# Optimization experiments

Hardware: AMD Instinct MI355X
Metric: run time of the kernel (lower is better)

Reference implementation:

```python
import jax, jax.numpy as jnp
import numpy as np

OUT_W, OUT_L, OUT_H = 7, 7, 7   # output_size
SR = 2                          # sampling_ratio (samples per bin per axis)


def setup_inputs() -> dict:
    key = jax.random.key(0)
    k1, k2, k3, k4, k5 = jax.random.split(key, 5)
    B, C, W, L, H = 2, 128, 64, 64, 64
    N = 128
    inp = jax.random.normal(k1, (B, C, W, L, H), jnp.float32)
    bidx = jax.random.randint(k2, (N,), 0, B).astype(jnp.float32)
    ctr = jax.random.uniform(k3, (N, 3), minval=8.0, maxval=56.0)
    size = jax.random.uniform(k4, (N, 3), minval=8.0, maxval=32.0)
    theta = jax.random.uniform(k5, (N, 1), minval=-np.pi, maxval=np.pi)
    rois = jnp.concatenate([bidx[:, None], ctr, size, theta], axis=1)  # [N,8]
    return {"input": inp, "rois": rois, "spatial_scale": jnp.float32(1.0)}


def _trilinear_gather(vol, b, x, y, z):
    # vol: [B,W,L,H,C]; b: [N]; x,y,z: [N,PW,PL,PH] float coords.
    B, W, L, H, C = vol.shape
    valid = (x > -1.0) & (x < W) & (y > -1.0) & (y < L) & (z > -1.0) & (z < H)
    x = jnp.clip(x, 0.0, W - 1.0)
    y = jnp.clip(y, 0.0, L - 1.0)
    z = jnp.clip(z, 0.0, H - 1.0)
    x0 = jnp.floor(x).astype(jnp.int32)
    y0 = jnp.floor(y).astype(jnp.int32)
    z0 = jnp.floor(z).astype(jnp.int32)
    x1 = jnp.minimum(x0 + 1, W - 1)
    y1 = jnp.minimum(y0 + 1, L - 1)
    z1 = jnp.minimum(z0 + 1, H - 1)
    lx = x - x0; hx = 1.0 - lx
    ly = y - y0; hy = 1.0 - ly
    lz = z - z0; hz = 1.0 - lz
    bb = b[:, None, None, None]

    def g(xi, yi, zi):
        return vol[bb, xi, yi, zi]  # [N,PW,PL,PH,C]

    out = (g(x0, y0, z0) * (hx * hy * hz)[..., None]
           + g(x1, y0, z0) * (lx * hy * hz)[..., None]
           + g(x0, y1, z0) * (hx * ly * hz)[..., None]
           + g(x1, y1, z0) * (lx * ly * hz)[..., None]
           + g(x0, y0, z1) * (hx * hy * lz)[..., None]
           + g(x1, y0, z1) * (lx * hy * lz)[..., None]
           + g(x0, y1, z1) * (hx * ly * lz)[..., None]
           + g(x1, y1, z1) * (lx * ly * lz)[..., None])
    return out * valid[..., None]


def _axis_offsets(size, nbins):
    # size: [N]; returns [N, nbins*SR] local coords centered at 0.
    binw = size / nbins
    i = jnp.arange(nbins * SR, dtype=jnp.float32)
    return (-size * 0.5)[:, None] + (i[None, :] + 0.5) * (binw / SR)[:, None]


def roi_align_rotated_3d(input, rois, spatial_scale):
    B, C, W, L, H = input.shape
    vol = jnp.transpose(input, (0, 2, 3, 4, 1))  # [B,W,L,H,C]
    b = rois[:, 0].astype(jnp.int32)
    ctr = rois[:, 1:4] * spatial_scale           # cx,cy,cz
    size = rois[:, 4:7] * spatial_scale          # w,l,h
    theta = rois[:, 7]
    N = rois.shape[0]

    xx = _axis_offsets(size[:, 0], OUT_W)[:, :, None, None]  # [N,PW,1,1]
    yy = _axis_offsets(size[:, 1], OUT_L)[:, None, :, None]  # [N,1,PL,1]
    zz = _axis_offsets(size[:, 2], OUT_H)[:, None, None, :]  # [N,1,1,PH]

    c = jnp.cos(theta)[:, None, None, None]
    s = jnp.sin(theta)[:, None, None, None]
    # rotate sample offsets about z-axis, then shift to ROI center
    x = c * xx - s * yy + ctr[:, 0][:, None, None, None]
    y = s * xx + c * yy + ctr[:, 1][:, None, None, None]
    z = jnp.broadcast_to(zz + ctr[:, 2][:, None, None, None],
                         (N, OUT_W * SR, OUT_L * SR, OUT_H * SR))
    x = jnp.broadcast_to(x, z.shape)
    y = jnp.broadcast_to(y, z.shape)

    vals = _trilinear_gather(vol, b, x, y, z)  # [N,PW,PL,PH,C]
    vals = vals.reshape(N, OUT_W, SR, OUT_L, SR, OUT_H, SR, C)
    pooled = vals.mean(axis=(2, 4, 6))          # [N,OW,OL,OH,C]
    return jnp.transpose(pooled, (0, 4, 1, 2, 3))  # [N,C,OW,OL,OH]


def reference(input, rois, spatial_scale):
    return roi_align_rotated_3d(input, rois, spatial_scale)
```

## Files before the change

kernel.cpp:

```cpp
#include <hip/hip_runtime.h>

#define OUT_W 7
#define OUT_L 7
#define OUT_H 7
#define SR 2
#define CDIM 128
#define WDIM 64
#define LDIM 64
#define HDIM 64
#define VOLSZ (WDIM * LDIM * HDIM)
#define CPB 2

typedef float f4 __attribute__((ext_vector_type(4)));

#define GLOAD(dst, p) asm volatile("global_load_dwordx4 %0, %1, off" : "=v"(dst) : "v"(p))

struct ColInfo { int b00, b10, b01, b11; float w00, w10, w01, w11; };

__global__ __launch_bounds__(384) void roi_align_rot3d_kernel(
    const float* __restrict__ input, const float* __restrict__ rois,
    const float* __restrict__ scale_ptr, float* __restrict__ out, int N)
{
    __shared__ ColInfo cols[OUT_W * SR * OUT_L * SR];
    __shared__ alignas(16) float zw[OUT_H][8];
    __shared__ int zb4s[OUT_H];

    const int nwg = N * (CDIM / CPB);
    const int q = nwg >> 3, rr = nwg & 7;
    const int xcd = blockIdx.x & 7;
    const int idx_in = blockIdx.x >> 3;
    const int w = (xcd < rr ? xcd * (q + 1) : rr * (q + 1) + (xcd - rr) * q) + idx_in;
    const int cp = w / N;
    const int n  = w - cp * N;
    const int c0 = cp * CPB;
    const int t = threadIdx.x;

    const float scale = scale_ptr[0];
    const float* r = rois + (size_t)n * 8;
    const int   b  = (int)r[0];
    const float cx = r[1] * scale, cy = r[2] * scale, cz = r[3] * scale;
    const float sx = r[4] * scale, sy = r[5] * scale, szv = r[6] * scale;
    const float th = r[7];
    const float ct = cosf(th), st = sinf(th);

    if (t < 196) {
        const int isx = t / 14, isy = t - isx * 14;
        const float xx = -0.5f * sx + ((float)isx + 0.5f) * (sx * (1.0f / 14.0f));
        const float yy = -0.5f * sy + ((float)isy + 0.5f) * (sy * (1.0f / 14.0f));
        float x = ct * xx - st * yy + cx;
        float y = st * xx + ct * yy + cy;
        const bool v = (x > -1.0f) && (x < (float)WDIM) && (y > -1.0f) && (y < (float)LDIM);
        x = fminf(fmaxf(x, 0.0f), (float)(WDIM - 1));
        y = fminf(fmaxf(y, 0.0f), (float)(LDIM - 1));
        const int x0 = (int)floorf(x);
        const int y0 = (int)floorf(y);
        const int x1 = min(x0 + 1, WDIM - 1);
        const int y1 = min(y0 + 1, LDIM - 1);
        const float lx = x - (float)x0, ly = y - (float)y0;
        const float hx = 1.0f - lx, hy = 1.0f - ly;
        const float vm = v ? 1.0f : 0.0f;
        cols[t].b00 = x0 * (LDIM * HDIM) + y0 * HDIM;
        cols[t].b10 = x1 * (LDIM * HDIM) + y0 * HDIM;
        cols[t].b01 = x0 * (LDIM * HDIM) + y1 * HDIM;
        cols[t].b11 = x1 * (LDIM * HDIM) + y1 * HDIM;
        cols[t].w00 = hx * hy * vm; cols[t].w10 = lx * hy * vm;
        cols[t].w01 = hx * ly * vm; cols[t].w11 = lx * ly * vm;
    } else if (t < 196 + OUT_H) {
        const int oh = t - 196;
        float w8[8];
        #pragma unroll
        for (int k = 0; k < 8; ++k) w8[k] = 0.0f;
        int zb4 = 0;
        #pragma unroll
        for (int dz = 0; dz < 2; ++dz) {
            const int s = oh * 2 + dz;
            const float zraw = -0.5f * szv + ((float)s + 0.5f) * (szv * (1.0f / 14.0f)) + cz;
            const bool v = (zraw > -1.0f) && (zraw < (float)HDIM);
            const float z = fminf(fmaxf(zraw, 0.0f), (float)(HDIM - 1));
            const int z0 = (int)floorf(z);
            const int z1 = min(z0 + 1, HDIM - 1);
            const float lz = z - (float)z0, hz = 1.0f - lz;
            const float vm = v ? 1.0f : 0.0f;
            if (dz == 0) zb4 = min(z0 & ~3, HDIM - 8);
            w8[z0 - zb4] += hz * vm;
            w8[z1 - zb4] += lz * vm;
        }
        zb4s[oh] = zb4;
        #pragma unroll
        for (int k = 0; k < 8; ++k) zw[oh][k] = w8[k];
    }
    __syncthreads();

    if (t >= 343) return;
    const int ow = t / 49;
    const int rem = t - ow * 49;
    const int ol = rem / 7;
    const int oh = rem - ol * 7;

    const float4 zwa = *(const float4*)&zw[oh][0];
    const float4 zwb = *(const float4*)&zw[oh][4];
    const int zb4 = zb4s[oh];

    const float* __restrict__ p =
        input + ((size_t)(b * CDIM + c0)) * (size_t)VOLSZ;

    float acc0 = 0.0f, acc1 = 0.0f;

    #pragma unroll
    for (int dx = 0; dx < 2; ++dx) {
        #pragma unroll
        for (int dy = 0; dy < 2; ++dy) {
            const ColInfo col = cols[(ow * 2 + dx) * 14 + (ol * 2 + dy)];
            const float* a0 = p + (col.b00 + zb4);
            const float* a1 = p + (col.b10 + zb4);
            const float* a2 = p + (col.b01 + zb4);
            const float* a3 = p + (col.b11 + zb4);
            const float* b0 = a0 + VOLSZ;
            const float* b1 = a1 + VOLSZ;
            const float* b2 = a2 + VOLSZ;
            const float* b3 = a3 + VOLSZ;
            f4 r00, r01, r02, r03, r04, r05, r06, r07;
            f4 r08, r09, r10, r11, r12, r13, r14, r15;
            GLOAD(r00, a0); GLOAD(r01, a0 + 4);
            GLOAD(r02, a1); GLOAD(r03, a1 + 4);
            GLOAD(r04, a2); GLOAD(r05, a2 + 4);
            GLOAD(r06, a3); GLOAD(r07, a3 + 4);
            GLOAD(r08, b0); GLOAD(r09, b0 + 4);
            GLOAD(r10, b1); GLOAD(r11, b1 + 4);
            GLOAD(r12, b2); GLOAD(r13, b2 + 4);
            GLOAD(r14, b3); GLOAD(r15, b3 + 4);
            asm volatile("s_waitcnt vmcnt(0)"
                : "+v"(r00), "+v"(r01), "+v"(r02), "+v"(r03),
                  "+v"(r04), "+v"(r05), "+v"(r06), "+v"(r07),
                  "+v"(r08), "+v"(r09), "+v"(r10), "+v"(r11),
                  "+v"(r12), "+v"(r13), "+v"(r14), "+v"(r15));
            const float v00 = zwa.x*r00.x + zwa.y*r00.y + zwa.z*r00.z + zwa.w*r00.w
                            + zwb.x*r01.x + zwb.y*r01.y + zwb.z*r01.z + zwb.w*r01.w;
            const float v10 = zwa.x*r02.x + zwa.y*r02.y + zwa.z*r02.z + zwa.w*r02.w
                            + zwb.x*r03.x + zwb.y*r03.y + zwb.z*r03.z + zwb.w*r03.w;
            const float v01 = zwa.x*r04.x + zwa.y*r04.y + zwa.z*r04.z + zwa.w*r04.w
                            + zwb.x*r05.x + zwb.y*r05.y + zwb.z*r05.z + zwb.w*r05.w;
            const float v11 = zwa.x*r06.x + zwa.y*r06.y + zwa.z*r06.z + zwa.w*r06.w
                            + zwb.x*r07.x + zwb.y*r07.y + zwb.z*r07.z + zwb.w*r07.w;
            acc0 += col.w00 * v00 + col.w10 * v10 + col.w01 * v01 + col.w11 * v11;
            const float u00 = zwa.x*r08.x + zwa.y*r08.y + zwa.z*r08.z + zwa.w*r08.w
                            + zwb.x*r09.x + zwb.y*r09.y + zwb.z*r09.z + zwb.w*r09.w;
            const float u10 = zwa.x*r10.x + zwa.y*r10.y + zwa.z*r10.z + zwa.w*r10.w
                            + zwb.x*r11.x + zwb.y*r11.y + zwb.z*r11.z + zwb.w*r11.w;
            const float u01 = zwa.x*r12.x + zwa.y*r12.y + zwa.z*r12.z + zwa.w*r12.w
                            + zwb.x*r13.x + zwb.y*r13.y + zwb.z*r13.z + zwb.w*r13.w;
            const float u11 = zwa.x*r14.x + zwa.y*r14.y + zwa.z*r14.z + zwa.w*r14.w
                            + zwb.x*r15.x + zwb.y*r15.y + zwb.z*r15.z + zwb.w*r15.w;
            acc1 += col.w00 * u00 + col.w10 * u10 + col.w01 * u01 + col.w11 * u11;
        }
    }
    out[((size_t)(n * CDIM + c0 + 0)) * 343 + t] = acc0 * 0.125f;
    out[((size_t)(n * CDIM + c0 + 1)) * 343 + t] = acc1 * 0.125f;
}

extern "C" void kernel_launch(void* const* d_in, const int* in_sizes, int n_in,
                              void* d_out, int out_size, void* d_ws, size_t ws_size,
                              hipStream_t stream) {
    const float* input = (const float*)d_in[0];
    const float* rois  = (const float*)d_in[1];
    const float* scale = (const float*)d_in[2];
    float* out = (float*)d_out;
    const int N = in_sizes[1] / 8;
    dim3 grid((unsigned)(N * (CDIM / CPB)));
    dim3 block(384);
    hipLaunchKernelGGL(roi_align_rot3d_kernel, grid, block, 0, stream,
                       input, rois, scale, out, N);
}
```

Before: 458.7 us.

## Stage xy-interpolated z-columns in LDS to share loads across output depths

Splits the kernel into two phases. First, each of the 196 xy sample columns loads the whole z range the ROI needs for two channels once, applies the bilinear xy weights, and writes the blended column to shared memory. Second, each output thread applies its z weights by reading from shared memory. This removes the repeated global loads that previously fetched overlapping z windows once per output depth bin. The cost is about 80 KB of LDS per block, which can limit the CU to one resident block and leave few waves to hide latency. It also adds a second barrier and a loop whose length depends on the ROI size, with a full wait in every iteration.

```diff
diff --git a/kernel.cpp b/kernel.cpp
--- a/kernel.cpp
+++ b/kernel.cpp
@@ -10,18 +10,29 @@
 #define HDIM 64
 #define VOLSZ (WDIM * LDIM * HDIM)
 #define CPB 2
+#define NSAMP (OUT_W * SR * OUT_L * SR)
+#define CSTRIDE 52
 
 typedef float f4 __attribute__((ext_vector_type(4)));
 
-#define GLOAD(dst, p) asm volatile("global_load_dwordx4 %0, %1, off" : "=v"(dst) : "v"(p))
+#define GLOAD(dst, p)   asm volatile("global_load_dwordx4 %0, %1, off"           : "=v"(dst) : "v"(p))
+#define GLOADO(dst, p)  asm volatile("global_load_dwordx4 %0, %1, off offset:16" : "=v"(dst) : "v"(p))
 
-struct ColInfo { int b00, b10, b01, b11; float w00, w10, w01, w11; };
+static __device__ __forceinline__ f4 interp4(float w00, float w10, float w01, float w11,
+                                             f4 a, f4 b, f4 c, f4 d) {
+    f4 o;
+    o.x = w00*a.x + w10*b.x + w01*c.x + w11*d.x;
+    o.y = w00*a.y + w10*b.y + w01*c.y + w11*d.y;
+    o.z = w00*a.z + w10*b.z + w01*c.z + w11*d.z;
+    o.w = w00*a.w + w10*b.w + w01*c.w + w11*d.w;
+    return o;
+}
 
 __global__ __launch_bounds__(384) void roi_align_rot3d_kernel(
     const float* __restrict__ input, const float* __restrict__ rois,
     const float* __restrict__ scale_ptr, float* __restrict__ out, int N)
 {
-    __shared__ ColInfo cols[OUT_W * SR * OUT_L * SR];
+    __shared__ alignas(16) float icol[CPB][NSAMP][CSTRIDE];
     __shared__ alignas(16) float zw[OUT_H][8];
     __shared__ int zb4s[OUT_H];
 
@@ -29,9 +40,9 @@
     const int q = nwg >> 3, rr = nwg & 7;
     const int xcd = blockIdx.x & 7;
     const int idx_in = blockIdx.x >> 3;
-    const int w = (xcd < rr ? xcd * (q + 1) : rr * (q + 1) + (xcd - rr) * q) + idx_in;
-    const int cp = w / N;
-    const int n  = w - cp * N;
+    const int wk = (xcd < rr ? xcd * (q + 1) : rr * (q + 1) + (xcd - rr) * q) + idx_in;
+    const int cp = wk / N;
+    const int n  = wk - cp * N;
     const int c0 = cp * CPB;
     const int t = threadIdx.x;
 
@@ -43,7 +54,10 @@
     const float th = r[7];
     const float ct = cosf(th), st = sinf(th);
 
-    if (t < 196) {
+    int b00 = 0, b10 = 0, b01 = 0, b11 = 0;
+    float w00 = 0.f, w10 = 0.f, w01 = 0.f, w11 = 0.f;
+
+    if (t < NSAMP) {
         const int isx = t / 14, isy = t - isx * 14;
         const float xx = -0.5f * sx + ((float)isx + 0.5f) * (sx * (1.0f / 14.0f));
         const float yy = -0.5f * sy + ((float)isy + 0.5f) * (sy * (1.0f / 14.0f));
@@ -59,14 +73,14 @@
         const float lx = x - (float)x0, ly = y - (float)y0;
         const float hx = 1.0f - lx, hy = 1.0f - ly;
         const float vm = v ? 1.0f : 0.0f;
-        cols[t].b00 = x0 * (LDIM * HDIM) + y0 * HDIM;
-        cols[t].b10 = x1 * (LDIM * HDIM) + y0 * HDIM;
-        cols[t].b01 = x0 * (LDIM * HDIM) + y1 * HDIM;
-        cols[t].b11 = x1 * (LDIM * HDIM) + y1 * HDIM;
-        cols[t].w00 = hx * hy * vm; cols[t].w10 = lx * hy * vm;
-        cols[t].w01 = hx * ly * vm; cols[t].w11 = lx * ly * vm;
-    } else if (t < 196 + OUT_H) {
-        const int oh = t - 196;
+        b00 = x0 * (LDIM * HDIM) + y0 * HDIM;
+        b10 = x1 * (LDIM * HDIM) + y0 * HDIM;
+        b01 = x0 * (LDIM * HDIM) + y1 * HDIM;
+        b11 = x1 * (LDIM * HDIM) + y1 * HDIM;
+        w00 = hx * hy * vm; w10 = lx * hy * vm;
+        w01 = hx * ly * vm; w11 = lx * ly * vm;
+    } else if (t < NSAMP + OUT_H) {
+        const int oh = t - NSAMP;
         float w8[8];
         #pragma unroll
         for (int k = 0; k < 8; ++k) w8[k] = 0.0f;
@@ -91,67 +105,73 @@
     }
     __syncthreads();
 
+    int zbase = zb4s[0];
+    int nch = ((zb4s[6] + 8) - zbase) >> 2;
+    if (nch & 1) { if (zbase >= 4) zbase -= 4; nch += 1; }
+    const int npairs = nch >> 1;
+
+    if (t < NSAMP) {
+        const float* base = input + (size_t)(b * CDIM + c0) * (size_t)VOLSZ + zbase;
+        const float* p00 = base + b00;
+        const float* p10 = base + b10;
+        const float* p01 = base + b01;
+        const float* p11 = base + b11;
+        const float* q00 = p00 + VOLSZ;
+        const float* q10 = p10 + VOLSZ;
+        const float* q01 = p01 + VOLSZ;
+        const float* q11 = p11 + VOLSZ;
+        float* l0 = &icol[0][t][0];
+        float* l1 = &icol[1][t][0];
+        for (int kp = 0; kp < npairs; ++kp) {
+            f4 r00, r01, r02, r03, r04, r05, r06, r07;
+            f4 r08, r09, r10, r11, r12, r13, r14, r15;
+            GLOAD(r00, p00); GLOADO(r01, p00);
+            GLOAD(r02, p10); GLOADO(r03, p10);
+            GLOAD(r04, p01); GLOADO(r05, p01);
+            GLOAD(r06, p11); GLOADO(r07, p11);
+            GLOAD(r08, q00); GLOADO(r09, q00);
+            GLOAD(r10, q10); GLOADO(r11, q10);
+            GLOAD(r12, q01); GLOADO(r13, q01);
+            GLOAD(r14, q11); GLOADO(r15, q11);
+            asm volatile("s_waitcnt vmcnt(0)"
+                : "+v"(r00), "+v"(r01), "+v"(r02), "+v"(r03),
+                  "+v"(r04), "+v"(r05), "+v"(r06), "+v"(r07),
+                  "+v"(r08), "+v"(r09), "+v"(r10), "+v"(r11),
+                  "+v"(r12), "+v"(r13), "+v"(r14), "+v"(r15));
+            *(f4*)(l0 + 8 * kp)     = interp4(w00, w10, w01, w11, r00, r02, r04, r06);
+            *(f4*)(l0 + 8 * kp + 4) = interp4(w00, w10, w01, w11, r01, r03, r05, r07);
+            *(f4*)(l1 + 8 * kp)     = interp4(w00, w10, w01, w11, r08, r10, r12, r14);
+            *(f4*)(l1 + 8 * kp + 4) = interp4(w00, w10, w01, w11, r09, r11, r13, r15);
+            p00 += 8; p10 += 8; p01 += 8; p11 += 8;
+            q00 += 8; q10 += 8; q01 += 8; q11 += 8;
+        }
+    }
+    __syncthreads();
+
     if (t >= 343) return;
     const int ow = t / 49;
     const int rem = t - ow * 49;
     const int ol = rem / 7;
     const int oh = rem - ol * 7;
 
-    const float4 zwa = *(const float4*)&zw[oh][0];
-    const float4 zwb = *(const float4*)&zw[oh][4];
-    const int zb4 = zb4s[oh];
-
-    const float* __restrict__ p =
-        input + ((size_t)(b * CDIM + c0)) * (size_t)VOLSZ;
+    const f4 zwa = *(const f4*)&zw[oh][0];
+    const f4 zwb = *(const f4*)&zw[oh][4];
+    const int off = zb4s[oh] - zbase;
 
     float acc0 = 0.0f, acc1 = 0.0f;
-
     #pragma unroll
     for (int dx = 0; dx < 2; ++dx) {
         #pragma unroll
         for (int dy = 0; dy < 2; ++dy) {
-            const ColInfo col = cols[(ow * 2 + dx) * 14 + (ol * 2 + dy)];
-            const float* a0 = p + (col.b00 + zb4);
-            const float* a1 = p + (col.b10 + zb4);
-            const float* a2 = p + (col.b01 + zb4);
-            const float* a3 = p + (col.b11 + zb4);
-            const float* b0 = a0 + VOLSZ;
-            const float* b1 = a1 + VOLSZ;
-            const float* b2 = a2 + VOLSZ;
-            const float* b3 = a3 + VOLSZ;
-            f4 r00, r01, r02, r03, r04, r05, r06, r07;
-            f4 r08, r09, r10, r11, r12, r13, r14, r15;
-            GLOAD(r00, a0); GLOAD(r01, a0 + 4);
-            GLOAD(r02, a1); GLOAD(r03, a1 + 4);
-            GLOAD(r04, a2); GLOAD(r05, a2 + 4);
-            GLOAD(r06, a3); GLOAD(r07, a3 + 4);
-            GLOAD(r08, b0); GLOAD(r09, b0 + 4);
-            GLOAD(r10, b1); GLOAD(r11, b1 + 4);
-            GLOAD(r12, b2); GLOAD(r13, b2 + 4);
-            GLOAD(r14, b3); GLOAD(r15, b3 + 4);
-            asm volatile("s_waitcnt vmcnt(0)"
-                : "+v"(r00), "+v"(r01), "+v"(r02), "+v"(r03),
-                  "+v"(r04), "+v"(r05), "+v"(r06), "+v"(r07),
-                  "+v"(r08), "+v"(r09), "+v"(r10), "+v"(r11),
-                  "+v"(r12), "+v"(r13), "+v"(r14), "+v"(r15));
-            const float v00 = zwa.x*r00.x + zwa.y*r00.y + zwa.z*r00.z + zwa.w*r00.w
-                            + zwb.x*r01.x + zwb.y*r01.y + zwb.z*r01.z + zwb.w*r01.w;
-            const float v10 = zwa.x*r02.x + zwa.y*r02.y + zwa.z*r02.z + zwa.w*r02.w
-                            + zwb.x*r03.x + zwb.y*r03.y + zwb.z*r03.z + zwb.w*r03.w;
-            const float v01 = zwa.x*r04.x + zwa.y*r04.y + zwa.z*r04.z + zwa.w*r04.w
-                            + zwb.x*r05.x + zwb.y*r05.y + zwb.z*r05.z + zwb.w*r05.w;
-            const float v11 = zwa.x*r06.x + zwa.y*r06.y + zwa.z*r06.z + zwa.w*r06.w
-                            + zwb.x*r07.x + zwb.y*r07.y + zwb.z*r07.z + zwb.w*r07.w;
-            acc0 += col.w00 * v00 + col.w10 * v10 + col.w01 * v01 + col.w11 * v11;
-            const float u00 = zwa.x*r08.x + zwa.y*r08.y + zwa.z*r08.z + zwa.w*r08.w
-                            + zwb.x*r09.x + zwb.y*r09.y + zwb.z*r09.z + zwb.w*r09.w;
-            const float u10 = zwa.x*r10.x + zwa.y*r10.y + zwa.z*r10.z + zwa.w*r10.w
-                            + zwb.x*r11.x + zwb.y*r11.y + zwb.z*r11.z + zwb.w*r11.w;
-            const float u01 = zwa.x*r12.x + zwa.y*r12.y + zwa.z*r12.z + zwa.w*r12.w
-                            + zwb.x*r13.x + zwb.y*r13.y + zwb.z*r13.z + zwb.w*r13.w;
-            const float u11 = zwa.x*r14.x + zwa.y*r14.y + zwa.z*r14.z + zwa.w*r14.w
-                            + zwb.x*r15.x + zwb.y*r15.y + zwb.z*r15.z + zwb.w*r15.w;
-            acc1 += col.w00 * u00 + col.w10 * u10 + col.w01 * u01 + col.w11 * u11;
+            const int s = (ow * 2 + dx) * 14 + (ol * 2 + dy);
+            const f4 va = *(const f4*)&icol[0][s][off];
+            const f4 vb = *(const f4*)&icol[0][s][off + 4];
+            acc0 += zwa.x*va.x + zwa.y*va.y + zwa.z*va.z + zwa.w*va.w
+                  + zwb.x*vb.x + zwb.y*vb.y + zwb.z*vb.z + zwb.w*vb.w;
+            const f4 ua = *(const f4*)&icol[1][s][off];
+            const f4 ub = *(const f4*)&icol[1][s][off + 4];
+            acc1 += zwa.x*ua.x + zwa.y*ua.y + zwa.z*ua.z + zwa.w*ua.w
+                  + zwb.x*ub.x + zwb.y*ub.y + zwb.z*ub.z + zwb.w*ub.w;
         }
     }
     out[((size_t)(n * CDIM + c0 + 0)) * 343 + t] = acc0 * 0.125f;
```

Measured after the change: 581.2 us. 1.27x slower.
